# Kernel optimization log

Measured on AMD Instinct MI355X. Metric: run time of the kernel, lower is better.

The kernel has to match this reference:

```python
import jax, jax.numpy as jnp
import numpy as np

N = 50000
E = 800000
IN_DIM = 256
HID = 256
OUT_DIM = 2


def setup_inputs() -> dict:
    key = jax.random.key(0)
    ks = jax.random.split(key, 10)
    x = jax.random.normal(ks[0], (N, IN_DIM), dtype=jnp.float32)
    edge_index = jax.random.randint(ks[1], (2, E), 0, N, dtype=jnp.int64)
    # Glorot-ish scaling so activations stay well-conditioned through 4 layers
    def w(k, fan_in, fan_out):
        return jax.random.normal(k, (fan_in, fan_out), dtype=jnp.float32) / jnp.sqrt(jnp.float32(fan_in))
    return {
        "x": x,
        "edge_index": edge_index,
        "W0": w(ks[2], IN_DIM, HID), "b0": jnp.zeros((HID,), jnp.float32),
        "W1": w(ks[3], HID, HID),    "b1": jnp.zeros((HID,), jnp.float32),
        "W2": w(ks[4], HID, HID),    "b2": jnp.zeros((HID,), jnp.float32),
        "W3": w(ks[5], HID, OUT_DIM), "b3": jnp.zeros((OUT_DIM,), jnp.float32),
    }


def _gcn_norm(edge_index, n, dtype):
    # PyG gcn_norm with self-loops: deg over destination, norm = d^-1/2[src]*d^-1/2[dst]
    loops = jnp.arange(n, dtype=edge_index.dtype)
    src = jnp.concatenate([edge_index[0], loops])
    dst = jnp.concatenate([edge_index[1], loops])
    deg = jax.ops.segment_sum(jnp.ones_like(dst, dtype=dtype), dst, num_segments=n)
    dis = deg ** -0.5  # deg >= 1 due to self-loops
    norm = dis[src] * dis[dst]
    return src, dst, norm


def reference(x, edge_index, W0, b0, W1, b1, W2, b2, W3, b3):
    n = x.shape[0]
    src, dst, norm = _gcn_norm(edge_index, n, x.dtype)

    def conv(h, W, b):
        h = h @ W                              # [N, F_out] dense GEMM
        msg = h[src] * norm[:, None]           # edge-gather + scale
        agg = jax.ops.segment_sum(msg, dst, num_segments=n)  # scatter-add
        return agg + b

    h = jax.nn.relu(conv(x, W0, b0))
    h = jax.nn.relu(conv(h, W1, b1))
    h = jax.nn.relu(conv(h, W2, b2))
    return conv(h, W3, b3)
```

## Files before the change

### kernel.cpp

```cpp
#include <hip/hip_runtime.h>

#define N_NODES 50000
#define N_EDGES 800000

static inline int cdiv(int a, int b) { return (a + b - 1) / b; }

typedef __attribute__((ext_vector_type(8))) short bf16x8;
typedef __attribute__((ext_vector_type(4))) float f32x4;

static __device__ __forceinline__ unsigned short f2bf(float f) {
    unsigned int u = __float_as_uint(f);
    unsigned int r = (u + 0x7FFF + ((u >> 16) & 1)) >> 16;
    return (unsigned short)r;
}
static __device__ __forceinline__ float bf2f(unsigned short h) {
    return __uint_as_float((unsigned int)h << 16);
}
static __device__ __forceinline__ float bf_lo(unsigned int u) { return __uint_as_float(u << 16); }
static __device__ __forceinline__ float bf_hi(unsigned int u) { return __uint_as_float(u & 0xFFFF0000u); }

static __device__ __forceinline__ int logc(int p) {
    int pl = p & 63;
    return (p & ~63) + (pl & 3) * 16 + (pl >> 2);
}

static __device__ __forceinline__ void acc8(float* acc, uint4 v, float wgt) {
    acc[0] += wgt * bf_lo(v.x);
    acc[1] += wgt * bf_hi(v.x);
    acc[2] += wgt * bf_lo(v.y);
    acc[3] += wgt * bf_hi(v.y);
    acc[4] += wgt * bf_lo(v.z);
    acc[5] += wgt * bf_hi(v.z);
    acc[6] += wgt * bf_lo(v.w);
    acc[7] += wgt * bf_hi(v.w);
}


__global__ void k_count(const int* __restrict__ edst, int* cnt, int e) {
    int i = blockIdx.x * 256 + threadIdx.x;
    if (i < e) atomicAdd(&cnt[edst[i]], 1);
}

__global__ __launch_bounds__(256) void k_scan1(const int* __restrict__ cnt,
                                               int* __restrict__ row_ptr,
                                               float* __restrict__ dis,
                                               int* __restrict__ blk, int n) {
    __shared__ int sums[256];
    int t = threadIdx.x;
    int base = blockIdx.x * 1024 + t * 4;
    int c0 = 0, c1 = 0, c2 = 0, c3 = 0;
    if (base + 3 < n) {
        int4 v = *(const int4*)(cnt + base);
        c0 = v.x + 1; c1 = v.y + 1; c2 = v.z + 1; c3 = v.w + 1;
    } else {
        if (base + 0 < n) c0 = cnt[base + 0] + 1;
        if (base + 1 < n) c1 = cnt[base + 1] + 1;
        if (base + 2 < n) c2 = cnt[base + 2] + 1;
        if (base + 3 < n) c3 = cnt[base + 3] + 1;
    }
    int s = c0 + c1 + c2 + c3;
    sums[t] = s;
    __syncthreads();
    int x = s;
    for (int off = 1; off < 256; off <<= 1) {
        int y = (t >= off) ? sums[t - off] : 0;
        __syncthreads();
        x += y;
        sums[t] = x;
        __syncthreads();
    }
    int excl = x - s;
    if (base + 0 < n) { row_ptr[base + 0] = excl;                dis[base + 0] = rsqrtf((float)c0); }
    if (base + 1 < n) { row_ptr[base + 1] = excl + c0;           dis[base + 1] = rsqrtf((float)c1); }
    if (base + 2 < n) { row_ptr[base + 2] = excl + c0 + c1;      dis[base + 2] = rsqrtf((float)c2); }
    if (base + 3 < n) { row_ptr[base + 3] = excl + c0 + c1 + c2; dis[base + 3] = rsqrtf((float)c3); }
    if (t == 255) blk[blockIdx.x] = x;
}

__global__ __launch_bounds__(256) void k_scan2(int* __restrict__ blk,
                                               int* __restrict__ row_ptr_n, int nb) {
    __shared__ int sums[256];
    int t = threadIdx.x;
    int s = (t < nb) ? blk[t] : 0;
    sums[t] = s;
    __syncthreads();
    int x = s;
    for (int off = 1; off < 256; off <<= 1) {
        int y = (t >= off) ? sums[t - off] : 0;
        __syncthreads();
        x += y;
        sums[t] = x;
        __syncthreads();
    }
    if (t < nb) blk[t] = x - s;
    if (t == 255) row_ptr_n[0] = x;
}

__global__ __launch_bounds__(256) void k_scan3(int* __restrict__ row_ptr,
                                               int* __restrict__ pos,
                                               const int* __restrict__ blk, int n) {
    int base = blockIdx.x * 1024 + threadIdx.x * 4;
    int off = blk[blockIdx.x];
#pragma unroll
    for (int i = 0; i < 4; ++i) {
        int idx = base + i;
        if (idx < n) {
            int v = row_ptr[idx] + off;
            row_ptr[idx] = v;
            pos[idx] = v;
        }
    }
}

__global__ void k_fill(const int* __restrict__ esrc, const int* __restrict__ edst,
                       int* pos, const float* __restrict__ dis,
                       int2* __restrict__ eg, int e, int n) {
    int i = blockIdx.x * 256 + threadIdx.x;
    if (i < e) {
        int s = esrc[i], d = edst[i];
        int p = atomicAdd(&pos[d], 1);
        eg[p] = make_int2(s, __float_as_int(dis[s] * dis[d]));
    } else if (i < e + n) {
        int v = i - e;
        int p = atomicAdd(&pos[v], 1);
        float dv = dis[v];
        eg[p] = make_int2(v, __float_as_int(dv * dv));
    }
}


__global__ __launch_bounds__(256) void k_prep(const float* __restrict__ W0,
                                              const float* __restrict__ W1,
                                              const float* __restrict__ W2,
                                              unsigned short* __restrict__ Wth,
                                              unsigned short* __restrict__ Wtl,
                                              const float* __restrict__ X,
                                              unsigned short* __restrict__ Xh, long total4) {
    if (blockIdx.x < 768) {
        int layer = blockIdx.x >> 8;
        int n = blockIdx.x & 255;
        int p = threadIdx.x;
        const float* W = layer == 0 ? W0 : (layer == 1 ? W1 : W2);
        int k = (layer != 0) ? logc(p) : p;
        float v = W[(size_t)k * 256 + n];
        unsigned short h = f2bf(v);
        size_t o = (size_t)layer * 65536 + (size_t)n * 256 + p;
        Wth[o] = h;
        Wtl[o] = f2bf(v - bf2f(h));
    } else {
        long i = (long)(blockIdx.x - 768) * 256 + threadIdx.x;
        if (i >= total4) return;
        float4 v = *(const float4*)(X + i * 4);
        ushort4 h;
        h.x = f2bf(v.x);
        h.y = f2bf(v.y);
        h.z = f2bf(v.z);
        h.w = f2bf(v.w);
        *(ushort4*)(Xh + i * 4) = h;
    }
}


#define GEMM_RB 196

__global__ __launch_bounds__(256) void k_gemm_mfma(const unsigned short* __restrict__ Ah,
                                                   const unsigned short* __restrict__ Wth,
                                                   const unsigned short* __restrict__ Wtl,
                                                   unsigned short* __restrict__ C, int M) {
    __shared__ unsigned short Wh[64][264];
    __shared__ unsigned short Wl[64][136];
    int rowblk = blockIdx.x % GEMM_RB;
    int colblk = blockIdx.x / GEMM_RB;
    int c0 = colblk * 64;
    int m0 = rowblk * 256;
    int t = threadIdx.x;
    int sr = t >> 2;

    {
        int hk0 = (t & 3) * 64;
        const unsigned short* gh = Wth + (size_t)(c0 + sr) * 256 + hk0;
        unsigned short* lh = &Wh[sr][hk0];
#pragma unroll
        for (int i = 0; i < 8; ++i)
            *(uint4*)(lh + i * 8) = *(const uint4*)(gh + i * 8);
        int lk0 = (t & 3) * 32;
        const unsigned short* gl = Wtl + (size_t)(c0 + sr) * 256 + lk0;
        unsigned short* ll = &Wl[sr][lk0];
#pragma unroll
        for (int i = 0; i < 4; ++i)
            *(uint4*)(ll + i * 8) = *(const uint4*)(gl + i * 8);
    }
    __syncthreads();

    int lane = t & 63, wave = t >> 6;
    int quad = lane >> 4, l16 = lane & 15;

    const unsigned short* aph[4];
#pragma unroll
    for (int mt = 0; mt < 4; ++mt) {
        int m = m0 + wave * 64 + mt * 16 + l16;
        if (m >= M) m = M - 1;
        aph[mt] = Ah + (size_t)m * 256 + quad * 8;
    }

    f32x4 acc[4][4];
#pragma unroll
    for (int i = 0; i < 4; ++i)
#pragma unroll
        for (int j = 0; j < 4; ++j) acc[i][j] = (f32x4){0.f, 0.f, 0.f, 0.f};

#pragma unroll 2
    for (int kc = 0; kc < 4; ++kc) {
        int ko = kc * 32;
        bf16x8 ahf[4];
#pragma unroll
        for (int mt = 0; mt < 4; ++mt) ahf[mt] = *(const bf16x8*)(aph[mt] + ko);
#pragma unroll
        for (int nt = 0; nt < 4; ++nt) {
            bf16x8 bh = *(const bf16x8*)&Wh[nt * 16 + l16][ko + quad * 8];
            bf16x8 bl = *(const bf16x8*)&Wl[nt * 16 + l16][ko + quad * 8];
#pragma unroll
            for (int mt = 0; mt < 4; ++mt) {
                acc[mt][nt] = __builtin_amdgcn_mfma_f32_16x16x32_bf16(ahf[mt], bh, acc[mt][nt], 0, 0, 0);
                acc[mt][nt] = __builtin_amdgcn_mfma_f32_16x16x32_bf16(ahf[mt], bl, acc[mt][nt], 0, 0, 0);
            }
        }
    }

    __syncthreads();
    {
        int lk0 = (t & 3) * 32;
        const unsigned short* gl = Wtl + (size_t)(c0 + sr) * 256 + 128 + lk0;
        unsigned short* ll = &Wl[sr][lk0];
#pragma unroll
        for (int i = 0; i < 4; ++i)
            *(uint4*)(ll + i * 8) = *(const uint4*)(gl + i * 8);
    }
    __syncthreads();

#pragma unroll 2
    for (int kc = 4; kc < 8; ++kc) {
        int ko = kc * 32;
        int kol = ko - 128;
        bf16x8 ahf[4];
#pragma unroll
        for (int mt = 0; mt < 4; ++mt) ahf[mt] = *(const bf16x8*)(aph[mt] + ko);
#pragma unroll
        for (int nt = 0; nt < 4; ++nt) {
            bf16x8 bh = *(const bf16x8*)&Wh[nt * 16 + l16][ko + quad * 8];
            bf16x8 bl = *(const bf16x8*)&Wl[nt * 16 + l16][kol + quad * 8];
#pragma unroll
            for (int mt = 0; mt < 4; ++mt) {
                acc[mt][nt] = __builtin_amdgcn_mfma_f32_16x16x32_bf16(ahf[mt], bh, acc[mt][nt], 0, 0, 0);
                acc[mt][nt] = __builtin_amdgcn_mfma_f32_16x16x32_bf16(ahf[mt], bl, acc[mt][nt], 0, 0, 0);
            }
        }
    }

#pragma unroll
    for (int mt = 0; mt < 4; ++mt) {
#pragma unroll
        for (int r = 0; r < 4; ++r) {
            int row = m0 + wave * 64 + mt * 16 + quad * 4 + r;
            if (row < M) {
                ushort4 sv;
                sv.x = f2bf(acc[mt][0][r]);
                sv.y = f2bf(acc[mt][1][r]);
                sv.z = f2bf(acc[mt][2][r]);
                sv.w = f2bf(acc[mt][3][r]);
                *(ushort4*)(C + (size_t)row * 256 + c0 + l16 * 4) = sv;
            }
        }
    }
}


__global__ __launch_bounds__(256) void k_agg256(const unsigned short* __restrict__ t,
                                                const int* __restrict__ row_ptr,
                                                const int2* __restrict__ eg,
                                                const float* __restrict__ bias,
                                                unsigned short* __restrict__ outh, int n) {
    int lane = threadIdx.x & 63;
    int wave = threadIdx.x >> 6;
    int node = blockIdx.x * 4 + wave;
    if (node >= n) return;
    int half = lane >> 5;
    int fl = lane & 31;
    int beg = row_ptr[node], end = row_ptr[node + 1];
    float acc[8] = {};
    const unsigned short* tp = t + fl * 8;

    int e = beg + half;
    for (; e + 6 < end; e += 8) {
        int2 a = eg[e], b = eg[e + 2], c = eg[e + 4], d = eg[e + 6];
        uint4 v0 = *(const uint4*)(tp + (size_t)a.x * 256);
        uint4 v1 = *(const uint4*)(tp + (size_t)b.x * 256);
        uint4 v2 = *(const uint4*)(tp + (size_t)c.x * 256);
        uint4 v3 = *(const uint4*)(tp + (size_t)d.x * 256);
        acc8(acc, v0, __int_as_float(a.y));
        acc8(acc, v1, __int_as_float(b.y));
        acc8(acc, v2, __int_as_float(c.y));
        acc8(acc, v3, __int_as_float(d.y));
    }
    for (; e + 2 < end; e += 4) {
        int2 a = eg[e], b = eg[e + 2];
        uint4 v0 = *(const uint4*)(tp + (size_t)a.x * 256);
        uint4 v1 = *(const uint4*)(tp + (size_t)b.x * 256);
        acc8(acc, v0, __int_as_float(a.y));
        acc8(acc, v1, __int_as_float(b.y));
    }
    if (e < end) {
        int2 a = eg[e];
        uint4 v0 = *(const uint4*)(tp + (size_t)a.x * 256);
        acc8(acc, v0, __int_as_float(a.y));
    }

#pragma unroll
    for (int i = 0; i < 8; ++i) acc[i] += __shfl_xor(acc[i], 32);

    if (half == 0) {
        ushort4 h0, h1;
#pragma unroll
        for (int j = 0; j < 8; ++j) {
            int cb = logc(fl * 8 + j);
            float v = acc[j] + bias[cb];
            v = v > 0.f ? v : 0.f;
            unsigned short h = f2bf(v);
            if (j == 0) h0.x = h;
            else if (j == 1) h0.y = h;
            else if (j == 2) h0.z = h;
            else if (j == 3) h0.w = h;
            else if (j == 4) h1.x = h;
            else if (j == 5) h1.y = h;
            else if (j == 6) h1.z = h;
            else h1.w = h;
        }
        unsigned short* oh = outh + (size_t)node * 256 + fl * 8;
        *(ushort4*)(oh + 0) = h0;
        *(ushort4*)(oh + 4) = h1;
    }
}


__global__ __launch_bounds__(256) void k_gemm_out2(const unsigned short* __restrict__ Hh,
                                                   const float* __restrict__ W3,
                                                   float* __restrict__ t2, int n) {
    int lane = threadIdx.x & 63;
    int wave = threadIdx.x >> 6;
    int row = blockIdx.x * 4 + wave;
    if (row >= n) return;
    ushort4 ah = *(const ushort4*)(Hh + (size_t)row * 256 + lane * 4);
    float v[4];
    v[0] = bf2f(ah.x);
    v[1] = bf2f(ah.y);
    v[2] = bf2f(ah.z);
    v[3] = bf2f(ah.w);
    float s0 = 0.f, s1 = 0.f;
#pragma unroll
    for (int i = 0; i < 4; ++i) {
        int c = logc(lane * 4 + i);
        float2 w = *(const float2*)(W3 + (size_t)c * 2);
        s0 += v[i] * w.x;
        s1 += v[i] * w.y;
    }
#pragma unroll
    for (int off = 32; off > 0; off >>= 1) {
        s0 += __shfl_down(s0, off);
        s1 += __shfl_down(s1, off);
    }
    if (lane == 0) {
        t2[(size_t)row * 2 + 0] = s0;
        t2[(size_t)row * 2 + 1] = s1;
    }
}

__global__ void k_agg2(const float* __restrict__ t2,
                       const int* __restrict__ row_ptr,
                       const int2* __restrict__ eg,
                       const float* __restrict__ b3,
                       float* __restrict__ out, int n) {
    int node = blockIdx.x * 256 + threadIdx.x;
    if (node >= n) return;
    int beg = row_ptr[node], end = row_ptr[node + 1];
    float a0 = 0.f, a1 = 0.f;
    for (int e = beg; e < end; ++e) {
        int2 m = eg[e];
        float w = __int_as_float(m.y);
        float2 v = *(const float2*)(t2 + (size_t)m.x * 2);
        a0 += w * v.x;
        a1 += w * v.y;
    }
    out[(size_t)node * 2 + 0] = a0 + b3[0];
    out[(size_t)node * 2 + 1] = a1 + b3[1];
}


extern "C" void kernel_launch(void* const* d_in, const int* in_sizes, int n_in,
                              void* d_out, int out_size, void* d_ws, size_t ws_size,
                              hipStream_t stream) {
    const int N = N_NODES, E = N_EDGES;
    const float* x  = (const float*)d_in[0];
    const int* ei   = (const int*)d_in[1];
    const int* esrc = ei;
    const int* edst = ei + E;
    const float* W0 = (const float*)d_in[2];
    const float* b0 = (const float*)d_in[3];
    const float* W1 = (const float*)d_in[4];
    const float* b1 = (const float*)d_in[5];
    const float* W2 = (const float*)d_in[6];
    const float* b2 = (const float*)d_in[7];
    const float* W3 = (const float*)d_in[8];
    const float* b3 = (const float*)d_in[9];
    float* out = (float*)d_out;

    unsigned short* Ahh = (unsigned short*)d_ws;
    unsigned short* Tb  = Ahh + (size_t)N * 256;
    unsigned short* Wth = Tb + (size_t)N * 256;
    unsigned short* Wtl = Wth + 3 * 65536;
    int2*  eg     = (int2*)(Wtl + 3 * 65536);
    float* t2     = (float*)(eg + (E + N));
    float* dis    = t2 + (size_t)N * 2;
    int*   cnt    = (int*)(dis + N);
    int*   row_ptr= cnt + N;
    int*   pos    = row_ptr + (N + 1);
    int*   blk    = pos + N;

    const int NB = cdiv(N, 1024);

    hipMemsetAsync(cnt, 0, (size_t)N * sizeof(int), stream);
    k_count<<<cdiv(E, 256), 256, 0, stream>>>(edst, cnt, E);
    k_scan1<<<NB, 256, 0, stream>>>(cnt, row_ptr, dis, blk, N);
    k_scan2<<<1, 256, 0, stream>>>(blk, row_ptr + N, NB);
    k_scan3<<<NB, 256, 0, stream>>>(row_ptr, pos, blk, N);
    k_fill<<<cdiv(E + N, 256), 256, 0, stream>>>(esrc, edst, pos, dis, eg, E, N);

    const int ggrid = GEMM_RB * 4;
    const int agrid = cdiv(N, 4);
    const long total4 = (long)N * 64;
    const int CA = cdiv((int)total4, 256);

    k_prep<<<768 + CA, 256, 0, stream>>>(W0, W1, W2, Wth, Wtl, x, Ahh, total4);

    k_gemm_mfma<<<ggrid, 256, 0, stream>>>(Ahh, Wth, Wtl, Tb, N);
    k_agg256<<<agrid, 256, 0, stream>>>(Tb, row_ptr, eg, b0, Ahh, N);
    k_gemm_mfma<<<ggrid, 256, 0, stream>>>(Ahh, Wth + 65536, Wtl + 65536, Tb, N);
    k_agg256<<<agrid, 256, 0, stream>>>(Tb, row_ptr, eg, b1, Ahh, N);
    k_gemm_mfma<<<ggrid, 256, 0, stream>>>(Ahh, Wth + 2 * 65536, Wtl + 2 * 65536, Tb, N);
    k_agg256<<<agrid, 256, 0, stream>>>(Tb, row_ptr, eg, b2, Ahh, N);
    k_gemm_out2<<<agrid, 256, 0, stream>>>(Ahh, W3, t2, N);
    k_agg2<<<cdiv(N, 256), 256, 0, stream>>>(t2, row_ptr, eg, b3, out, N);
}
```

Before: 473.1 us.

## Fuse final projection into last aggregation and tune gather/scatter kernels

Fuses the 256->2 output projection into the third aggregation kernel so the layer-3 activations are never written and reread. It also adds a prepared permuted bias/W3 buffer, nontemporal loads and stores for edge data, a deeper unroll (12 edges) with packed f32x2 FMAs in the aggregation, vectorized edge counting, and four threads per node in the final 2-wide aggregation. Together these target memory traffic and per-node latency, at the cost of more register pressure from the wider unroll.

```diff
diff --git a/kernel.cpp b/kernel.cpp
--- a/kernel.cpp
+++ b/kernel.cpp
@@ -7,6 +7,8 @@
 
 typedef __attribute__((ext_vector_type(8))) short bf16x8;
 typedef __attribute__((ext_vector_type(4))) float f32x4;
+typedef __attribute__((ext_vector_type(2))) float f32x2;
+typedef __attribute__((ext_vector_type(4))) unsigned int u32x4;
 
 static __device__ __forceinline__ unsigned short f2bf(float f) {
     unsigned int u = __float_as_uint(f);
@@ -24,21 +26,37 @@
     return (p & ~63) + (pl & 3) * 16 + (pl >> 2);
 }
 
-static __device__ __forceinline__ void acc8(float* acc, uint4 v, float wgt) {
-    acc[0] += wgt * bf_lo(v.x);
-    acc[1] += wgt * bf_hi(v.x);
-    acc[2] += wgt * bf_lo(v.y);
-    acc[3] += wgt * bf_hi(v.y);
-    acc[4] += wgt * bf_lo(v.z);
-    acc[5] += wgt * bf_hi(v.z);
-    acc[6] += wgt * bf_lo(v.w);
-    acc[7] += wgt * bf_hi(v.w);
+static __device__ __forceinline__ int2 ldnt2(const int2* p) {
+    unsigned long long u = __builtin_nontemporal_load((const unsigned long long*)p);
+    int2 r;
+    r.x = (int)(u & 0xFFFFFFFFull);
+    r.y = (int)(u >> 32);
+    return r;
+}
+
+static __device__ __forceinline__ void acc8p(f32x2* acc, uint4 v, float wgt) {
+    f32x2 w2;
+    w2.x = wgt;
+    w2.y = wgt;
+    f32x2 p;
+    p.x = bf_lo(v.x); p.y = bf_hi(v.x); acc[0] += p * w2;
+    p.x = bf_lo(v.y); p.y = bf_hi(v.y); acc[1] += p * w2;
+    p.x = bf_lo(v.z); p.y = bf_hi(v.z); acc[2] += p * w2;
+    p.x = bf_lo(v.w); p.y = bf_hi(v.w); acc[3] += p * w2;
 }
 
 
 __global__ void k_count(const int* __restrict__ edst, int* cnt, int e) {
-    int i = blockIdx.x * 256 + threadIdx.x;
-    if (i < e) atomicAdd(&cnt[edst[i]], 1);
+    int i = (blockIdx.x * 256 + threadIdx.x) * 4;
+    if (i + 3 < e) {
+        int4 v = *(const int4*)(edst + i);
+        atomicAdd(&cnt[v.x], 1);
+        atomicAdd(&cnt[v.y], 1);
+        atomicAdd(&cnt[v.z], 1);
+        atomicAdd(&cnt[v.w], 1);
+    } else {
+        for (int k = i; k < e; ++k) atomicAdd(&cnt[edst[k]], 1);
+    }
 }
 
 __global__ __launch_bounds__(256) void k_scan1(const int* __restrict__ cnt,
@@ -119,12 +137,16 @@
     if (i < e) {
         int s = esrc[i], d = edst[i];
         int p = atomicAdd(&pos[d], 1);
-        eg[p] = make_int2(s, __float_as_int(dis[s] * dis[d]));
+        unsigned long long u = (unsigned long long)(unsigned int)s |
+                               ((unsigned long long)(unsigned int)__float_as_int(dis[s] * dis[d]) << 32);
+        __builtin_nontemporal_store(u, (unsigned long long*)&eg[p]);
     } else if (i < e + n) {
         int v = i - e;
         int p = atomicAdd(&pos[v], 1);
         float dv = dis[v];
-        eg[p] = make_int2(v, __float_as_int(dv * dv));
+        unsigned long long u = (unsigned long long)(unsigned int)v |
+                               ((unsigned long long)(unsigned int)__float_as_int(dv * dv) << 32);
+        __builtin_nontemporal_store(u, (unsigned long long*)&eg[p]);
     }
 }
 
@@ -132,8 +154,13 @@
 __global__ __launch_bounds__(256) void k_prep(const float* __restrict__ W0,
                                               const float* __restrict__ W1,
                                               const float* __restrict__ W2,
+                                              const float* __restrict__ b0,
+                                              const float* __restrict__ b1,
+                                              const float* __restrict__ b2,
+                                              const float* __restrict__ W3,
                                               unsigned short* __restrict__ Wth,
                                               unsigned short* __restrict__ Wtl,
+                                              float* __restrict__ bpw,
                                               const float* __restrict__ X,
                                               unsigned short* __restrict__ Xh, long total4) {
     if (blockIdx.x < 768) {
@@ -147,8 +174,16 @@
         size_t o = (size_t)layer * 65536 + (size_t)n * 256 + p;
         Wth[o] = h;
         Wtl[o] = f2bf(v - bf2f(h));
+    } else if (blockIdx.x == 768) {
+        int p = threadIdx.x;
+        int c = logc(p);
+        bpw[p] = b0[c];
+        bpw[256 + p] = b1[c];
+        bpw[512 + p] = b2[c];
+        bpw[768 + p * 2 + 0] = W3[(size_t)c * 2 + 0];
+        bpw[768 + p * 2 + 1] = W3[(size_t)c * 2 + 1];
     } else {
-        long i = (long)(blockIdx.x - 768) * 256 + threadIdx.x;
+        long i = (long)(blockIdx.x - 769) * 256 + threadIdx.x;
         if (i >= total4) return;
         float4 v = *(const float4*)(X + i * 4);
         ushort4 h;
@@ -275,11 +310,14 @@
 }
 
 
-__global__ __launch_bounds__(256) void k_agg256(const unsigned short* __restrict__ t,
-                                                const int* __restrict__ row_ptr,
-                                                const int2* __restrict__ eg,
-                                                const float* __restrict__ bias,
-                                                unsigned short* __restrict__ outh, int n) {
+template <int MODE>
+__global__ __launch_bounds__(256, 8) void k_agg256(const unsigned short* __restrict__ t,
+                                                   const int* __restrict__ row_ptr,
+                                                   const int2* __restrict__ eg,
+                                                   const float* __restrict__ bp,
+                                                   unsigned short* __restrict__ outh,
+                                                   const float* __restrict__ w3p,
+                                                   float* __restrict__ t2, int n) {
     int lane = threadIdx.x & 63;
     int wave = threadIdx.x >> 6;
     int node = blockIdx.x * 4 + wave;
@@ -287,111 +325,129 @@
     int half = lane >> 5;
     int fl = lane & 31;
     int beg = row_ptr[node], end = row_ptr[node + 1];
-    float acc[8] = {};
+    f32x2 acc2[4];
+#pragma unroll
+    for (int i = 0; i < 4; ++i) { acc2[i].x = 0.f; acc2[i].y = 0.f; }
     const unsigned short* tp = t + fl * 8;
 
     int e = beg + half;
+    for (; e + 10 < end; e += 12) {
+        int2 a0 = ldnt2(eg + e), a1 = ldnt2(eg + e + 2), a2 = ldnt2(eg + e + 4);
+        int2 a3 = ldnt2(eg + e + 6), a4 = ldnt2(eg + e + 8), a5 = ldnt2(eg + e + 10);
+        uint4 v0 = *(const uint4*)(tp + (size_t)a0.x * 256);
+        uint4 v1 = *(const uint4*)(tp + (size_t)a1.x * 256);
+        uint4 v2 = *(const uint4*)(tp + (size_t)a2.x * 256);
+        uint4 v3 = *(const uint4*)(tp + (size_t)a3.x * 256);
+        uint4 v4 = *(const uint4*)(tp + (size_t)a4.x * 256);
+        uint4 v5 = *(const uint4*)(tp + (size_t)a5.x * 256);
+        acc8p(acc2, v0, __int_as_float(a0.y));
+        acc8p(acc2, v1, __int_as_float(a1.y));
+        acc8p(acc2, v2, __int_as_float(a2.y));
+        acc8p(acc2, v3, __int_as_float(a3.y));
+        acc8p(acc2, v4, __int_as_float(a4.y));
+        acc8p(acc2, v5, __int_as_float(a5.y));
+    }
     for (; e + 6 < end; e += 8) {
-        int2 a = eg[e], b = eg[e + 2], c = eg[e + 4], d = eg[e + 6];
-        uint4 v0 = *(const uint4*)(tp + (size_t)a.x * 256);
-        uint4 v1 = *(const uint4*)(tp + (size_t)b.x * 256);
-        uint4 v2 = *(const uint4*)(tp + (size_t)c.x * 256);
-        uint4 v3 = *(const uint4*)(tp + (size_t)d.x * 256);
-        acc8(acc, v0, __int_as_float(a.y));
-        acc8(acc, v1, __int_as_float(b.y));
-        acc8(acc, v2, __int_as_float(c.y));
-        acc8(acc, v3, __int_as_float(d.y));
+        int2 a0 = ldnt2(eg + e), a1 = ldnt2(eg + e + 2);
+        int2 a2 = ldnt2(eg + e + 4), a3 = ldnt2(eg + e + 6);
+        uint4 v0 = *(const uint4*)(tp + (size_t)a0.x * 256);
+        uint4 v1 = *(const uint4*)(tp + (size_t)a1.x * 256);
+        uint4 v2 = *(const uint4*)(tp + (size_t)a2.x * 256);
+        uint4 v3 = *(const uint4*)(tp + (size_t)a3.x * 256);
+        acc8p(acc2, v0, __int_as_float(a0.y));
+        acc8p(acc2, v1, __int_as_float(a1.y));
+        acc8p(acc2, v2, __int_as_float(a2.y));
+        acc8p(acc2, v3, __int_as_float(a3.y));
     }
     for (; e + 2 < end; e += 4) {
-        int2 a = eg[e], b = eg[e + 2];
-        uint4 v0 = *(const uint4*)(tp + (size_t)a.x * 256);
-        uint4 v1 = *(const uint4*)(tp + (size_t)b.x * 256);
-        acc8(acc, v0, __int_as_float(a.y));
-        acc8(acc, v1, __int_as_float(b.y));
+        int2 a0 = ldnt2(eg + e), a1 = ldnt2(eg + e + 2);
+        uint4 v0 = *(const uint4*)(tp + (size_t)a0.x * 256);
+        uint4 v1 = *(const uint4*)(tp + (size_t)a1.x * 256);
+        acc8p(acc2, v0, __int_as_float(a0.y));
+        acc8p(acc2, v1, __int_as_float(a1.y));
     }
     if (e < end) {
-        int2 a = eg[e];
-        uint4 v0 = *(const uint4*)(tp + (size_t)a.x * 256);
-        acc8(acc, v0, __int_as_float(a.y));
-    }
-
-#pragma unroll
-    for (int i = 0; i < 8; ++i) acc[i] += __shfl_xor(acc[i], 32);
-
-    if (half == 0) {
-        ushort4 h0, h1;
-#pragma unroll
-        for (int j = 0; j < 8; ++j) {
-            int cb = logc(fl * 8 + j);
-            float v = acc[j] + bias[cb];
-            v = v > 0.f ? v : 0.f;
-            unsigned short h = f2bf(v);
-            if (j == 0) h0.x = h;
-            else if (j == 1) h0.y = h;
-            else if (j == 2) h0.z = h;
-            else if (j == 3) h0.w = h;
-            else if (j == 4) h1.x = h;
-            else if (j == 5) h1.y = h;
-            else if (j == 6) h1.z = h;
-            else h1.w = h;
-        }
-        unsigned short* oh = outh + (size_t)node * 256 + fl * 8;
-        *(ushort4*)(oh + 0) = h0;
-        *(ushort4*)(oh + 4) = h1;
-    }
-}
-
-
-__global__ __launch_bounds__(256) void k_gemm_out2(const unsigned short* __restrict__ Hh,
-                                                   const float* __restrict__ W3,
-                                                   float* __restrict__ t2, int n) {
-    int lane = threadIdx.x & 63;
-    int wave = threadIdx.x >> 6;
-    int row = blockIdx.x * 4 + wave;
-    if (row >= n) return;
-    ushort4 ah = *(const ushort4*)(Hh + (size_t)row * 256 + lane * 4);
-    float v[4];
-    v[0] = bf2f(ah.x);
-    v[1] = bf2f(ah.y);
-    v[2] = bf2f(ah.z);
-    v[3] = bf2f(ah.w);
-    float s0 = 0.f, s1 = 0.f;
-#pragma unroll
-    for (int i = 0; i < 4; ++i) {
-        int c = logc(lane * 4 + i);
-        float2 w = *(const float2*)(W3 + (size_t)c * 2);
-        s0 += v[i] * w.x;
-        s1 += v[i] * w.y;
-    }
-#pragma unroll
-    for (int off = 32; off > 0; off >>= 1) {
-        s0 += __shfl_down(s0, off);
-        s1 += __shfl_down(s1, off);
-    }
-    if (lane == 0) {
-        t2[(size_t)row * 2 + 0] = s0;
-        t2[(size_t)row * 2 + 1] = s1;
-    }
-}
+        int2 a0 = ldnt2(eg + e);
+        uint4 v0 = *(const uint4*)(tp + (size_t)a0.x * 256);
+        acc8p(acc2, v0, __int_as_float(a0.y));
+    }
+
+    float va[8];
+#pragma unroll
+    for (int i = 0; i < 4; ++i) { va[2 * i] = acc2[i].x; va[2 * i + 1] = acc2[i].y; }
+#pragma unroll
+    for (int i = 0; i < 8; ++i) va[i] += __shfl_xor(va[i], 32);
+
+    if (MODE == 0) {
+        if (half == 0) {
+            float4 bA = *(const float4*)(bp + fl * 8);
+            float4 bB = *(const float4*)(bp + fl * 8 + 4);
+            float r0 = fmaxf(va[0] + bA.x, 0.f), r1 = fmaxf(va[1] + bA.y, 0.f);
+            float r2 = fmaxf(va[2] + bA.z, 0.f), r3 = fmaxf(va[3] + bA.w, 0.f);
+            float r4 = fmaxf(va[4] + bB.x, 0.f), r5 = fmaxf(va[5] + bB.y, 0.f);
+            float r6 = fmaxf(va[6] + bB.z, 0.f), r7 = fmaxf(va[7] + bB.w, 0.f);
+            u32x4 w;
+            w.x = (unsigned)f2bf(r0) | ((unsigned)f2bf(r1) << 16);
+            w.y = (unsigned)f2bf(r2) | ((unsigned)f2bf(r3) << 16);
+            w.z = (unsigned)f2bf(r4) | ((unsigned)f2bf(r5) << 16);
+            w.w = (unsigned)f2bf(r6) | ((unsigned)f2bf(r7) << 16);
+            __builtin_nontemporal_store(w, (u32x4*)(outh + (size_t)node * 256 + fl * 8));
+        }
+    } else {
+        float4 bA = *(const float4*)(bp + fl * 8);
+        float4 bB = *(const float4*)(bp + fl * 8 + 4);
+        float r0 = fmaxf(va[0] + bA.x, 0.f), r1 = fmaxf(va[1] + bA.y, 0.f);
+        float r2 = fmaxf(va[2] + bA.z, 0.f), r3 = fmaxf(va[3] + bA.w, 0.f);
+        float r4 = fmaxf(va[4] + bB.x, 0.f), r5 = fmaxf(va[5] + bB.y, 0.f);
+        float r6 = fmaxf(va[6] + bB.z, 0.f), r7 = fmaxf(va[7] + bB.w, 0.f);
+        const float* wp = w3p + fl * 16;
+        float4 wA = *(const float4*)(wp + 0);
+        float4 wB = *(const float4*)(wp + 4);
+        float4 wC = *(const float4*)(wp + 8);
+        float4 wD = *(const float4*)(wp + 12);
+        float s0 = r0 * wA.x + r1 * wA.z + r2 * wB.x + r3 * wB.z +
+                   r4 * wC.x + r5 * wC.z + r6 * wD.x + r7 * wD.z;
+        float s1 = r0 * wA.y + r1 * wA.w + r2 * wB.y + r3 * wB.w +
+                   r4 * wC.y + r5 * wC.w + r6 * wD.y + r7 * wD.w;
+#pragma unroll
+        for (int off = 16; off > 0; off >>= 1) {
+            s0 += __shfl_xor(s0, off);
+            s1 += __shfl_xor(s1, off);
+        }
+        if (lane == 0) {
+            f32x2 o;
+            o.x = s0;
+            o.y = s1;
+            __builtin_nontemporal_store(o, (f32x2*)(t2 + (size_t)node * 2));
+        }
+    }
+}
+
 
 __global__ void k_agg2(const float* __restrict__ t2,
                        const int* __restrict__ row_ptr,
                        const int2* __restrict__ eg,
                        const float* __restrict__ b3,
                        float* __restrict__ out, int n) {
-    int node = blockIdx.x * 256 + threadIdx.x;
+    int tid = blockIdx.x * 256 + threadIdx.x;
+    int node = tid >> 2;
+    int sub = tid & 3;
     if (node >= n) return;
     int beg = row_ptr[node], end = row_ptr[node + 1];
     float a0 = 0.f, a1 = 0.f;
-    for (int e = beg; e < end; ++e) {
-        int2 m = eg[e];
+    for (int e = beg + sub; e < end; e += 4) {
+        int2 m = ldnt2(eg + e);
         float w = __int_as_float(m.y);
         float2 v = *(const float2*)(t2 + (size_t)m.x * 2);
         a0 += w * v.x;
         a1 += w * v.y;
     }
-    out[(size_t)node * 2 + 0] = a0 + b3[0];
-    out[(size_t)node * 2 + 1] = a1 + b3[1];
+    a0 += __shfl_xor(a0, 1); a1 += __shfl_xor(a1, 1);
+    a0 += __shfl_xor(a0, 2); a1 += __shfl_xor(a1, 2);
+    if (sub == 0) {
+        out[(size_t)node * 2 + 0] = a0 + b3[0];
+        out[(size_t)node * 2 + 1] = a1 + b3[1];
+    }
 }
 
 
@@ -419,7 +475,8 @@
     unsigned short* Wtl = Wth + 3 * 65536;
     int2*  eg     = (int2*)(Wtl + 3 * 65536);
     float* t2     = (float*)(eg + (E + N));
-    float* dis    = t2 + (size_t)N * 2;
+    float* bpw    = t2 + (size_t)N * 2;
+    float* dis    = bpw + 1280;
     int*   cnt    = (int*)(dis + N);
     int*   row_ptr= cnt + N;
     int*   pos    = row_ptr + (N + 1);
@@ -428,7 +485,7 @@
     const int NB = cdiv(N, 1024);
 
     hipMemsetAsync(cnt, 0, (size_t)N * sizeof(int), stream);
-    k_count<<<cdiv(E, 256), 256, 0, stream>>>(edst, cnt, E);
+    k_count<<<cdiv(E, 1024), 256, 0, stream>>>(edst, cnt, E);
     k_scan1<<<NB, 256, 0, stream>>>(cnt, row_ptr, dis, blk, N);
     k_scan2<<<1, 256, 0, stream>>>(blk, row_ptr + N, NB);
     k_scan3<<<NB, 256, 0, stream>>>(row_ptr, pos, blk, N);
@@ -439,14 +496,13 @@
     const long total4 = (long)N * 64;
     const int CA = cdiv((int)total4, 256);
 
-    k_prep<<<768 + CA, 256, 0, stream>>>(W0, W1, W2, Wth, Wtl, x, Ahh, total4);
+    k_prep<<<769 + CA, 256, 0, stream>>>(W0, W1, W2, b0, b1, b2, W3, Wth, Wtl, bpw, x, Ahh, total4);
 
     k_gemm_mfma<<<ggrid, 256, 0, stream>>>(Ahh, Wth, Wtl, Tb, N);
-    k_agg256<<<agrid, 256, 0, stream>>>(Tb, row_ptr, eg, b0, Ahh, N);
+    k_agg256<0><<<agrid, 256, 0, stream>>>(Tb, row_ptr, eg, bpw, Ahh, nullptr, nullptr, N);
     k_gemm_mfma<<<ggrid, 256, 0, stream>>>(Ahh, Wth + 65536, Wtl + 65536, Tb, N);
-    k_agg256<<<agrid, 256, 0, stream>>>(Tb, row_ptr, eg, b1, Ahh, N);
+    k_agg256<0><<<agrid, 256, 0, stream>>>(Tb, row_ptr, eg, bpw + 256, Ahh, nullptr, nullptr, N);
     k_gemm_mfma<<<ggrid, 256, 0, stream>>>(Ahh, Wth + 2 * 65536, Wtl + 2 * 65536, Tb, N);
-    k_agg256<<<agrid, 256, 0, stream>>>(Tb, row_ptr, eg, b2, Ahh, N);
-    k_gemm_out2<<<agrid, 256, 0, stream>>>(Ahh, W3, t2, N);
-    k_agg2<<<cdiv(N, 256), 256, 0, stream>>>(t2, row_ptr, eg, b3, out, N);
-}
+    k_agg256<1><<<agrid, 256, 0, stream>>>(Tb, row_ptr, eg, bpw + 512, nullptr, bpw + 768, t2, N);
+    k_agg2<<<cdiv(4 * N, 256), 256, 0, stream>>>(t2, row_ptr, eg, b3, out, N);
+}
```

New measurement: 465.8 us. Within noise of the previous version (-1.5%).
